# Kernel optimization log

Measured on AMD Instinct MI355X. Metric: run time of the kernel, lower is better.

The kernel has to match this reference:

```python
import jax, jax.numpy as jnp
import numpy as np

BIAS_BOUND = 8.0

def setup_inputs() -> dict:
    key = jax.random.key(0)
    k1, k2, k3 = jax.random.split(key, 3)
    x = jax.random.normal(k1, (8192, 4096), dtype=jnp.float32)
    # original init: uniform(-1.5, 1.5) for weight, uniform(-bias_bound, bias_bound) for bias
    weight = jax.random.uniform(k2, (4096, 4096), dtype=jnp.float32, minval=-1.5, maxval=1.5)
    bias = jax.random.uniform(k3, (4096,), dtype=jnp.float32, minval=-BIAS_BOUND, maxval=BIAS_BOUND)
    return {"x": x, "weight": weight, "bias": bias}

def reference(x, weight, bias):
    # temperature = 0 path: hard ternary quantization of weights
    w = jnp.clip(jnp.sign(jnp.round(weight)), -1.0, 1.0)      # [out, in] in {-1,0,1}
    b = jnp.clip(jnp.round(bias), -BIAS_BOUND, BIAS_BOUND)    # integer-valued bias
    # F.linear: x @ w.T + b
    return jnp.einsum('ni,oi->no', x, w) + b
```

## Files before the change

### kernel.cpp

```cpp
#include <hip/hip_runtime.h>
#include <hip/hip_bf16.h>
#include <stdint.h>

typedef __bf16 bf16x8 __attribute__((ext_vector_type(8)));
typedef float f32x4 __attribute__((ext_vector_type(4)));

#define BM 128
#define BN 128
#define BK 32


__global__ void cvt_x_kernel(const float* __restrict__ in, __bf16* __restrict__ out,
                             size_t n8) {
    size_t i = (size_t)blockIdx.x * blockDim.x + threadIdx.x;
    size_t stride = (size_t)gridDim.x * blockDim.x;
    for (; i < n8; i += stride) {
        size_t base = i * 8;
        float4 f0 = *reinterpret_cast<const float4*>(in + base);
        float4 f1 = *reinterpret_cast<const float4*>(in + base + 4);
        bf16x8 o;
        o[0] = (__bf16)f0.x; o[1] = (__bf16)f0.y;
        o[2] = (__bf16)f0.z; o[3] = (__bf16)f0.w;
        o[4] = (__bf16)f1.x; o[5] = (__bf16)f1.y;
        o[6] = (__bf16)f1.z; o[7] = (__bf16)f1.w;
        *reinterpret_cast<bf16x8*>(out + base) = o;
    }
}

__global__ void cvt_w_kernel(const float* __restrict__ in, __bf16* __restrict__ out,
                             size_t n8) {
    size_t i = (size_t)blockIdx.x * blockDim.x + threadIdx.x;
    size_t stride = (size_t)gridDim.x * blockDim.x;
    for (; i < n8; i += stride) {
        size_t base = i * 8;
        float4 f0 = *reinterpret_cast<const float4*>(in + base);
        float4 f1 = *reinterpret_cast<const float4*>(in + base + 4);
        float f[8] = {f0.x, f0.y, f0.z, f0.w, f1.x, f1.y, f1.z, f1.w};
        bf16x8 o;
#pragma unroll
        for (int j = 0; j < 8; ++j) {
            float t = (f[j] > 0.5f) ? 1.0f : ((f[j] < -0.5f) ? -1.0f : 0.0f);
            o[j] = (__bf16)t;
        }
        *reinterpret_cast<bf16x8*>(out + base) = o;
    }
}


__global__ __launch_bounds__(256) void gemm_kernel(
    const __bf16* __restrict__ A, const __bf16* __restrict__ B,
    const float* __restrict__ bias, float* __restrict__ out,
    int M, int N, int K) {
    __shared__ __bf16 sA[BM][BK];
    __shared__ __bf16 sB[BN][BK];

    const int t    = threadIdx.x;
    const int lane = t & 63;
    const int wave = t >> 6;
    const int wm   = (wave >> 1) * 64;
    const int wn   = (wave & 1) * 64;
    const int fr   = lane & 15;
    const int kg   = lane >> 4;

    const int blockCol = blockIdx.x * BN;
    const int blockRow = blockIdx.y * BM;

    const int r4 = t >> 2;
    const int c8 = (t & 3) * 8;
    const __bf16* gA0 = A + (size_t)(blockRow + r4) * K + c8;
    const __bf16* gA1 = A + (size_t)(blockRow + 64 + r4) * K + c8;
    const __bf16* gB0 = B + (size_t)(blockCol + r4) * K + c8;
    const __bf16* gB1 = B + (size_t)(blockCol + 64 + r4) * K + c8;
    __bf16* lA0 = &sA[0][0] + (size_t)t * 8;
    __bf16* lA1 = lA0 + 64 * BK;
    __bf16* lB0 = &sB[0][0] + (size_t)t * 8;
    __bf16* lB1 = lB0 + 64 * BK;

    f32x4 acc[4][4] = {};

    for (int k0 = 0; k0 < K; k0 += BK) {
        __builtin_amdgcn_global_load_lds(
            (const __attribute__((address_space(1))) void*)(gA0 + k0),
            (__attribute__((address_space(3))) void*)lA0, 16, 0, 0);
        __builtin_amdgcn_global_load_lds(
            (const __attribute__((address_space(1))) void*)(gA1 + k0),
            (__attribute__((address_space(3))) void*)lA1, 16, 0, 0);
        __builtin_amdgcn_global_load_lds(
            (const __attribute__((address_space(1))) void*)(gB0 + k0),
            (__attribute__((address_space(3))) void*)lB0, 16, 0, 0);
        __builtin_amdgcn_global_load_lds(
            (const __attribute__((address_space(1))) void*)(gB1 + k0),
            (__attribute__((address_space(3))) void*)lB1, 16, 0, 0);
        __syncthreads();

        bf16x8 av[4], bv[4];
#pragma unroll
        for (int i = 0; i < 4; ++i)
            av[i] = *reinterpret_cast<const bf16x8*>(&sA[wm + i * 16 + fr][kg * 8]);
#pragma unroll
        for (int j = 0; j < 4; ++j)
            bv[j] = *reinterpret_cast<const bf16x8*>(&sB[wn + j * 16 + fr][kg * 8]);

#pragma unroll
        for (int i = 0; i < 4; ++i)
#pragma unroll
            for (int j = 0; j < 4; ++j)
                acc[i][j] = __builtin_amdgcn_mfma_f32_16x16x32_bf16(
                    av[i], bv[j], acc[i][j], 0, 0, 0);
        __syncthreads();
    }

#pragma unroll
    for (int j = 0; j < 4; ++j) {
        const int col = blockCol + wn + j * 16 + fr;
        const float bq = fminf(8.0f, fmaxf(-8.0f, rintf(bias[col])));
#pragma unroll
        for (int i = 0; i < 4; ++i) {
            const int row0 = blockRow + wm + i * 16 + kg * 4;
#pragma unroll
            for (int r = 0; r < 4; ++r) {
                out[(size_t)(row0 + r) * N + col] = acc[i][j][r] + bq;
            }
        }
    }
}

__global__ void naive_kernel(const float* __restrict__ X, const float* __restrict__ W,
                             const float* __restrict__ bias, float* __restrict__ out,
                             int M, int N, int K) {
    int n = blockIdx.x * 16 + (threadIdx.x & 15);
    int m = blockIdx.y * 16 + (threadIdx.x >> 4);
    if (m >= M || n >= N) return;
    float acc = 0.f;
    for (int k = 0; k < K; ++k) {
        float w = W[(size_t)n * K + k];
        float t = (w > 0.5f) ? 1.0f : ((w < -0.5f) ? -1.0f : 0.0f);
        acc += X[(size_t)m * K + k] * t;
    }
    float b = fminf(8.0f, fmaxf(-8.0f, rintf(bias[n])));
    out[(size_t)m * N + n] = acc + b;
}

extern "C" void kernel_launch(void* const* d_in, const int* in_sizes, int n_in,
                              void* d_out, int out_size, void* d_ws, size_t ws_size,
                              hipStream_t stream) {
    const float* x    = (const float*)d_in[0];
    const float* w    = (const float*)d_in[1];
    const float* bias = (const float*)d_in[2];
    float* out        = (float*)d_out;

    const int N = in_sizes[2];
    const int K = in_sizes[1] / N;
    const int M = in_sizes[0] / K;

    const size_t xb_elems = (size_t)M * K;
    const size_t wb_elems = (size_t)N * K;
    const size_t need = (xb_elems + wb_elems) * sizeof(__bf16);

    if (ws_size >= need && (M % BM == 0) && (N % BN == 0) && (K % BK == 0)) {
        __bf16* xb = (__bf16*)d_ws;
        __bf16* wb = xb + xb_elems;
        cvt_x_kernel<<<2048, 256, 0, stream>>>(x, xb, xb_elems / 8);
        cvt_w_kernel<<<1024, 256, 0, stream>>>(w, wb, wb_elems / 8);
        dim3 grid(N / BN, M / BM);
        gemm_kernel<<<grid, 256, 0, stream>>>(xb, wb, bias, out, M, N, K);
    } else {
        dim3 grid((N + 15) / 16, (M + 15) / 16);
        naive_kernel<<<grid, 256, 0, stream>>>(x, w, bias, out, M, N, K);
    }
}
```

Measured before the change: 619.7 us.

## Rewrite GEMM as 256x256 tile, 8-wave, double-buffered swizzled LDS pipeline

Replaces the 128x128 single-buffer GEMM with a 256x256 tile, 512-thread kernel. It uses a 64-wide K step, double-buffered 128KB LDS with XOR swizzling, and staged global-to-LDS prefetch interleaved with four MFMA phases under explicit waitcnt and barriers. It also adds XCD-aware block remapping and merges the two conversion kernels into one launch. The aim is to hide global load latency, cut LDS bank conflicts and raise MFMA utilization. In exchange it brings heavy register pressure, whole-LDS occupancy and fragile manual synchronization.

```diff
diff --git a/kernel.cpp b/kernel.cpp
--- a/kernel.cpp
+++ b/kernel.cpp
@@ -5,122 +5,190 @@
 typedef __bf16 bf16x8 __attribute__((ext_vector_type(8)));
 typedef float f32x4 __attribute__((ext_vector_type(4)));
 
-#define BM 128
-#define BN 128
-#define BK 32
-
-
-__global__ void cvt_x_kernel(const float* __restrict__ in, __bf16* __restrict__ out,
-                             size_t n8) {
+#define AS1 __attribute__((address_space(1)))
+#define AS3 __attribute__((address_space(3)))
+
+__global__ void cvt_kernel(const float* __restrict__ x, const float* __restrict__ w,
+                           __bf16* __restrict__ xb, __bf16* __restrict__ wb,
+                           size_t nx8, size_t ntot8) {
     size_t i = (size_t)blockIdx.x * blockDim.x + threadIdx.x;
     size_t stride = (size_t)gridDim.x * blockDim.x;
-    for (; i < n8; i += stride) {
-        size_t base = i * 8;
-        float4 f0 = *reinterpret_cast<const float4*>(in + base);
-        float4 f1 = *reinterpret_cast<const float4*>(in + base + 4);
-        bf16x8 o;
-        o[0] = (__bf16)f0.x; o[1] = (__bf16)f0.y;
-        o[2] = (__bf16)f0.z; o[3] = (__bf16)f0.w;
-        o[4] = (__bf16)f1.x; o[5] = (__bf16)f1.y;
-        o[6] = (__bf16)f1.z; o[7] = (__bf16)f1.w;
-        *reinterpret_cast<bf16x8*>(out + base) = o;
-    }
-}
-
-__global__ void cvt_w_kernel(const float* __restrict__ in, __bf16* __restrict__ out,
-                             size_t n8) {
-    size_t i = (size_t)blockIdx.x * blockDim.x + threadIdx.x;
-    size_t stride = (size_t)gridDim.x * blockDim.x;
-    for (; i < n8; i += stride) {
-        size_t base = i * 8;
-        float4 f0 = *reinterpret_cast<const float4*>(in + base);
-        float4 f1 = *reinterpret_cast<const float4*>(in + base + 4);
-        float f[8] = {f0.x, f0.y, f0.z, f0.w, f1.x, f1.y, f1.z, f1.w};
-        bf16x8 o;
-#pragma unroll
-        for (int j = 0; j < 8; ++j) {
-            float t = (f[j] > 0.5f) ? 1.0f : ((f[j] < -0.5f) ? -1.0f : 0.0f);
-            o[j] = (__bf16)t;
-        }
-        *reinterpret_cast<bf16x8*>(out + base) = o;
-    }
-}
-
-
-__global__ __launch_bounds__(256) void gemm_kernel(
+    for (; i < ntot8; i += stride) {
+        if (i < nx8) {
+            size_t base = i * 8;
+            float4 f0 = *reinterpret_cast<const float4*>(x + base);
+            float4 f1 = *reinterpret_cast<const float4*>(x + base + 4);
+            bf16x8 o;
+            o[0] = (__bf16)f0.x; o[1] = (__bf16)f0.y; o[2] = (__bf16)f0.z; o[3] = (__bf16)f0.w;
+            o[4] = (__bf16)f1.x; o[5] = (__bf16)f1.y; o[6] = (__bf16)f1.z; o[7] = (__bf16)f1.w;
+            *reinterpret_cast<bf16x8*>(xb + base) = o;
+        } else {
+            size_t base = (i - nx8) * 8;
+            float4 f0 = *reinterpret_cast<const float4*>(w + base);
+            float4 f1 = *reinterpret_cast<const float4*>(w + base + 4);
+            float f[8] = {f0.x, f0.y, f0.z, f0.w, f1.x, f1.y, f1.z, f1.w};
+            bf16x8 o;
+#pragma unroll
+            for (int j = 0; j < 8; ++j) {
+                float tv = (f[j] > 0.5f) ? 1.0f : ((f[j] < -0.5f) ? -1.0f : 0.0f);
+                o[j] = (__bf16)tv;
+            }
+            *reinterpret_cast<bf16x8*>(wb + base) = o;
+        }
+    }
+}
+
+
+#define GLOAD(srcp, dstoff) \
+    __builtin_amdgcn_global_load_lds((const AS1 void*)(srcp), \
+        (AS3 void*)(lds + (dstoff)), 16, 0, 0)
+
+#define STAGE_A0(DB, KT) do { GLOAD(srcA00 + (size_t)(KT)*64, (DB)*65536 +     0 + t*16); \
+                              GLOAD(srcA01 + (size_t)(KT)*64, (DB)*65536 +  8192 + t*16); } while(0)
+#define STAGE_A1(DB, KT) do { GLOAD(srcA10 + (size_t)(KT)*64, (DB)*65536 + 16384 + t*16); \
+                              GLOAD(srcA11 + (size_t)(KT)*64, (DB)*65536 + 24576 + t*16); } while(0)
+#define STAGE_B0(DB, KT) do { GLOAD(srcB00 + (size_t)(KT)*64, (DB)*65536 + 32768 + t*16); \
+                              GLOAD(srcB01 + (size_t)(KT)*64, (DB)*65536 + 40960 + t*16); } while(0)
+#define STAGE_B1(DB, KT) do { GLOAD(srcB10 + (size_t)(KT)*64, (DB)*65536 + 49152 + t*16); \
+                              GLOAD(srcB11 + (size_t)(KT)*64, (DB)*65536 + 57344 + t*16); } while(0)
+
+#define LD8(off) (*(const bf16x8*)(lds + (off)))
+
+#define PHASE_SYNC_PRE() do { asm volatile("" ::: "memory"); \
+    __builtin_amdgcn_s_barrier(); \
+    asm volatile("s_waitcnt lgkmcnt(0)" ::: "memory"); \
+    __builtin_amdgcn_sched_barrier(0); } while(0)
+
+#define PHASE_SYNC_POST() do { __builtin_amdgcn_sched_barrier(0); \
+    asm volatile("" ::: "memory"); \
+    __builtin_amdgcn_s_barrier(); \
+    asm volatile("" ::: "memory"); } while(0)
+
+#define MFMA_QUAD(I0, J0) do { \
+    __builtin_amdgcn_s_setprio(1); \
+    _Pragma("unroll") for (int kk2 = 0; kk2 < 2; ++kk2) \
+    _Pragma("unroll") for (int ii2 = 0; ii2 < 4; ++ii2) \
+    _Pragma("unroll") for (int jj2 = 0; jj2 < 2; ++jj2) \
+        acc[(I0)+ii2][(J0)+jj2] = __builtin_amdgcn_mfma_f32_16x16x32_bf16( \
+            af[ii2][kk2], bfr[(J0)+jj2][kk2], acc[(I0)+ii2][(J0)+jj2], 0, 0, 0); \
+    __builtin_amdgcn_s_setprio(0); } while(0)
+
+__global__ __launch_bounds__(512, 2) void gemm_kernel(
     const __bf16* __restrict__ A, const __bf16* __restrict__ B,
     const float* __restrict__ bias, float* __restrict__ out,
     int M, int N, int K) {
-    __shared__ __bf16 sA[BM][BK];
-    __shared__ __bf16 sB[BN][BK];
+    __shared__ __align__(16) unsigned char lds[131072];
 
     const int t    = threadIdx.x;
     const int lane = t & 63;
     const int wave = t >> 6;
-    const int wm   = (wave >> 1) * 64;
-    const int wn   = (wave & 1) * 64;
+    const int wm   = wave >> 2;
+    const int wn   = wave & 3;
     const int fr   = lane & 15;
     const int kg   = lane >> 4;
-
-    const int blockCol = blockIdx.x * BN;
-    const int blockRow = blockIdx.y * BM;
-
-    const int r4 = t >> 2;
-    const int c8 = (t & 3) * 8;
-    const __bf16* gA0 = A + (size_t)(blockRow + r4) * K + c8;
-    const __bf16* gA1 = A + (size_t)(blockRow + 64 + r4) * K + c8;
-    const __bf16* gB0 = B + (size_t)(blockCol + r4) * K + c8;
-    const __bf16* gB1 = B + (size_t)(blockCol + 64 + r4) * K + c8;
-    __bf16* lA0 = &sA[0][0] + (size_t)t * 8;
-    __bf16* lA1 = lA0 + 64 * BK;
-    __bf16* lB0 = &sB[0][0] + (size_t)t * 8;
-    __bf16* lB1 = lB0 + 64 * BK;
-
-    f32x4 acc[4][4] = {};
-
-    for (int k0 = 0; k0 < K; k0 += BK) {
-        __builtin_amdgcn_global_load_lds(
-            (const __attribute__((address_space(1))) void*)(gA0 + k0),
-            (__attribute__((address_space(3))) void*)lA0, 16, 0, 0);
-        __builtin_amdgcn_global_load_lds(
-            (const __attribute__((address_space(1))) void*)(gA1 + k0),
-            (__attribute__((address_space(3))) void*)lA1, 16, 0, 0);
-        __builtin_amdgcn_global_load_lds(
-            (const __attribute__((address_space(1))) void*)(gB0 + k0),
-            (__attribute__((address_space(3))) void*)lB0, 16, 0, 0);
-        __builtin_amdgcn_global_load_lds(
-            (const __attribute__((address_space(1))) void*)(gB1 + k0),
-            (__attribute__((address_space(3))) void*)lB1, 16, 0, 0);
-        __syncthreads();
-
-        bf16x8 av[4], bv[4];
-#pragma unroll
-        for (int i = 0; i < 4; ++i)
-            av[i] = *reinterpret_cast<const bf16x8*>(&sA[wm + i * 16 + fr][kg * 8]);
-#pragma unroll
-        for (int j = 0; j < 4; ++j)
-            bv[j] = *reinterpret_cast<const bf16x8*>(&sB[wn + j * 16 + fr][kg * 8]);
-
-#pragma unroll
-        for (int i = 0; i < 4; ++i)
-#pragma unroll
-            for (int j = 0; j < 4; ++j)
-                acc[i][j] = __builtin_amdgcn_mfma_f32_16x16x32_bf16(
-                    av[i], bv[j], acc[i][j], 0, 0, 0);
-        __syncthreads();
+    const int NT   = K >> 6;
+
+    const int nwg  = gridDim.x * gridDim.y;
+    int flat = blockIdx.y * gridDim.x + blockIdx.x;
+    if ((nwg & 7) == 0) {
+        const int cpx = nwg >> 3;
+        flat = (flat & 7) * cpx + (flat >> 3);
+    }
+    const int blockCol = (flat % gridDim.x) * 256;
+    const int blockRow = (flat / gridDim.x) * 256;
+
+    const int tq  = t >> 3;
+    const int gce = ((t & 7) ^ (tq & 7)) * 8;
+    const __bf16* srcA00 = A + (size_t)(blockRow +   0 + tq) * K + gce;
+    const __bf16* srcA01 = A + (size_t)(blockRow + 128 + tq) * K + gce;
+    const __bf16* srcA10 = A + (size_t)(blockRow +  64 + tq) * K + gce;
+    const __bf16* srcA11 = A + (size_t)(blockRow + 192 + tq) * K + gce;
+    const int brB = (tq >> 5) * 64 + (tq & 31);
+    const __bf16* srcB00 = B + (size_t)(blockCol +       brB) * K + gce;
+    const __bf16* srcB01 = B + (size_t)(blockCol + 128 + brB) * K + gce;
+    const __bf16* srcB10 = B + (size_t)(blockCol +  32 + brB) * K + gce;
+    const __bf16* srcB11 = B + (size_t)(blockCol + 128 + 32 + brB) * K + gce;
+
+    int offA[8], offB[4];
+#pragma unroll
+    for (int i = 0; i < 8; ++i)
+        offA[i] = (((i >> 2) * 128 + wm * 64 + (i & 3) * 16 + fr) << 7);
+#pragma unroll
+    for (int j = 0; j < 4; ++j)
+        offB[j] = 32768 + ((((j >> 1) * 128 + wn * 32 + (j & 1) * 16 + fr)) << 7);
+    const int sw0 = ((kg ^ (fr & 7)) << 4);
+    const int sw1 = sw0 ^ 64;
+
+    f32x4 acc[8][4] = {};
+    bf16x8 af[4][2];
+    bf16x8 bfr[4][2];
+
+    STAGE_A0(0, 0); STAGE_A1(0, 0); STAGE_B0(0, 0); STAGE_B1(0, 0);
+    if (NT > 1) { STAGE_B0(1, 1); STAGE_A0(1, 1); STAGE_B1(1, 1); }
+    if (NT > 1) { asm volatile("s_waitcnt vmcnt(6)" ::: "memory"); }
+    else        { asm volatile("s_waitcnt vmcnt(0)" ::: "memory"); }
+    __builtin_amdgcn_s_barrier();
+    asm volatile("" ::: "memory");
+
+    for (int kt = 0; kt < NT; ++kt) {
+        const int db  = kt & 1;
+        const int dbB = db << 16;
+        const bool pf1 = (kt + 1 < NT);
+        const bool pf2 = (kt + 2 < NT);
+
+#pragma unroll
+        for (int ii = 0; ii < 4; ++ii) {
+            af[ii][0] = LD8(dbB + offA[ii] + sw0);
+            af[ii][1] = LD8(dbB + offA[ii] + sw1);
+        }
+#pragma unroll
+        for (int jj = 0; jj < 2; ++jj) {
+            bfr[jj][0] = LD8(dbB + offB[jj] + sw0);
+            bfr[jj][1] = LD8(dbB + offB[jj] + sw1);
+        }
+        if (pf1) STAGE_A1(db ^ 1, kt + 1);
+        PHASE_SYNC_PRE();
+        MFMA_QUAD(0, 0);
+        PHASE_SYNC_POST();
+
+#pragma unroll
+        for (int jj = 2; jj < 4; ++jj) {
+            bfr[jj][0] = LD8(dbB + offB[jj] + sw0);
+            bfr[jj][1] = LD8(dbB + offB[jj] + sw1);
+        }
+        if (pf2) STAGE_B0(db, kt + 2);
+        PHASE_SYNC_PRE();
+        MFMA_QUAD(0, 2);
+        PHASE_SYNC_POST();
+
+#pragma unroll
+        for (int ii = 0; ii < 4; ++ii) {
+            af[ii][0] = LD8(dbB + offA[ii + 4] + sw0);
+            af[ii][1] = LD8(dbB + offA[ii + 4] + sw1);
+        }
+        if (pf2) STAGE_A0(db, kt + 2);
+        PHASE_SYNC_PRE();
+        MFMA_QUAD(4, 2);
+        PHASE_SYNC_POST();
+
+        if (pf2) STAGE_B1(db, kt + 2);
+        if (pf2)      { asm volatile("s_waitcnt vmcnt(6)" ::: "memory"); }
+        else if (pf1) { asm volatile("s_waitcnt vmcnt(0)" ::: "memory"); }
+        PHASE_SYNC_PRE();
+        MFMA_QUAD(4, 0);
+        PHASE_SYNC_POST();
     }
 
 #pragma unroll
     for (int j = 0; j < 4; ++j) {
-        const int col = blockCol + wn + j * 16 + fr;
+        const int col = blockCol + wn * 64 + j * 16 + fr;
         const float bq = fminf(8.0f, fmaxf(-8.0f, rintf(bias[col])));
 #pragma unroll
-        for (int i = 0; i < 4; ++i) {
-            const int row0 = blockRow + wm + i * 16 + kg * 4;
-#pragma unroll
-            for (int r = 0; r < 4; ++r) {
+        for (int i = 0; i < 8; ++i) {
+            const int row0 = blockRow + wm * 128 + i * 16 + kg * 4;
+#pragma unroll
+            for (int r = 0; r < 4; ++r)
                 out[(size_t)(row0 + r) * N + col] = acc[i][j][r] + bq;
-            }
         }
     }
 }
@@ -134,8 +202,8 @@
     float acc = 0.f;
     for (int k = 0; k < K; ++k) {
         float w = W[(size_t)n * K + k];
-        float t = (w > 0.5f) ? 1.0f : ((w < -0.5f) ? -1.0f : 0.0f);
-        acc += X[(size_t)m * K + k] * t;
+        float tv = (w > 0.5f) ? 1.0f : ((w < -0.5f) ? -1.0f : 0.0f);
+        acc += X[(size_t)m * K + k] * tv;
     }
     float b = fminf(8.0f, fmaxf(-8.0f, rintf(bias[n])));
     out[(size_t)m * N + n] = acc + b;
@@ -157,13 +225,13 @@
     const size_t wb_elems = (size_t)N * K;
     const size_t need = (xb_elems + wb_elems) * sizeof(__bf16);
 
-    if (ws_size >= need && (M % BM == 0) && (N % BN == 0) && (K % BK == 0)) {
+    if (ws_size >= need && (M % 256 == 0) && (N % 256 == 0) && (K % 64 == 0) && K >= 192) {
         __bf16* xb = (__bf16*)d_ws;
         __bf16* wb = xb + xb_elems;
-        cvt_x_kernel<<<2048, 256, 0, stream>>>(x, xb, xb_elems / 8);
-        cvt_w_kernel<<<1024, 256, 0, stream>>>(w, wb, wb_elems / 8);
-        dim3 grid(N / BN, M / BM);
-        gemm_kernel<<<grid, 256, 0, stream>>>(xb, wb, bias, out, M, N, K);
+        cvt_kernel<<<4096, 256, 0, stream>>>(x, w, xb, wb, xb_elems / 8,
+                                             (xb_elems + wb_elems) / 8);
+        dim3 grid(N / 256, M / 256);
+        gemm_kernel<<<grid, 512, 0, stream>>>(xb, wb, bias, out, M, N, K);
     } else {
         dim3 grid((N + 15) / 16, (M + 15) / 16);
         naive_kernel<<<grid, 256, 0, stream>>>(x, w, bias, out, M, N, K);
```

Result: faster. 497.3 us (-19.7%).
